# Kernel optimization log

Hardware: AMD Instinct MI355X
Metric: run time of the kernel (lower is better)

Reference implementation:

```python
import jax, jax.numpy as jnp
import numpy as np

WS = 8          # window size
DIM = 512       # channels
NH = 16         # heads
HD = DIM // NH  # head dim = 32
N = WS * WS     # tokens per window = 64
NW = 64         # windows per image
B = 16          # images
BW = B * NW     # total windows = 1024
SCALE = HD ** -0.5


def _relative_position_index():
    # Swin relative position index, shape (N, N), values in [0, (2*WS-1)^2)
    coords = np.stack(np.meshgrid(np.arange(WS), np.arange(WS), indexing='ij'))  # (2, WS, WS)
    coords_flat = coords.reshape(2, -1)                                           # (2, N)
    rel = coords_flat[:, :, None] - coords_flat[:, None, :]                       # (2, N, N)
    rel = rel.transpose(1, 2, 0).astype(np.int32)                                 # (N, N, 2)
    rel[:, :, 0] += WS - 1
    rel[:, :, 1] += WS - 1
    rel[:, :, 0] *= 2 * WS - 1
    return jnp.asarray(rel.sum(-1))                                               # (N, N)


def setup_inputs() -> dict:
    key = jax.random.key(0)
    ks = jax.random.split(key, 7)
    x = jax.random.normal(ks[0], (BW, N, DIM), dtype=jnp.float32)
    mask = jax.random.normal(ks[1], (NW, N, N), dtype=jnp.float32)  # shift mask (additive)
    qkv_w = jax.random.normal(ks[2], (3 * DIM, DIM), dtype=jnp.float32) * 0.02
    qkv_b = jax.random.normal(ks[3], (3 * DIM,), dtype=jnp.float32) * 0.02
    rel_bias_table = jax.random.normal(ks[4], ((2 * WS - 1) ** 2, NH), dtype=jnp.float32) * 0.02
    proj_w = jax.random.normal(ks[5], (DIM, DIM), dtype=jnp.float32) * 0.02
    proj_b = jax.random.normal(ks[6], (DIM,), dtype=jnp.float32) * 0.02
    rel_index = _relative_position_index()
    return {"x": x, "mask": mask, "qkv_w": qkv_w, "qkv_b": qkv_b,
            "rel_bias_table": rel_bias_table, "proj_w": proj_w, "proj_b": proj_b,
            "rel_index": rel_index}


def reference(x, mask, qkv_w, qkv_b, rel_bias_table, proj_w, proj_b, rel_index):
    # qkv projection: (BW, N, 3*DIM) -> (3, BW, NH, N, HD)
    qkv = (x @ qkv_w.T + qkv_b).reshape(BW, N, 3, NH, HD).transpose(2, 0, 3, 1, 4)
    q, k, v = qkv[0], qkv[1], qkv[2]
    # scaled dot-product scores: (BW, NH, N, N)
    attn = jnp.einsum('bhnd,bhmd->bhnm', q * SCALE, k)
    # relative position bias: gather (N*N,) -> (N, N, NH) -> (NH, N, N)
    bias = rel_bias_table[rel_index.reshape(-1)].reshape(N, N, NH).transpose(2, 0, 1)
    attn = attn + bias[None]
    # shift mask: broadcast over images and heads
    attn = attn.reshape(B, NW, NH, N, N) + mask[None, :, None]
    attn = jax.nn.softmax(attn.reshape(BW, NH, N, N), axis=-1)
    # weighted values: (BW, NH, N, HD) -> (BW, N, DIM)
    out = jnp.einsum('bhnm,bhmd->bhnd', attn, v).transpose(0, 2, 1, 3).reshape(BW, N, DIM)
    return out @ proj_w.T + proj_b
```

## Files before the change

kernel.cpp:

```cpp
#include <hip/hip_runtime.h>
#include <hip/hip_bf16.h>

typedef __bf16 bf16;
typedef __bf16 bf16x4 __attribute__((ext_vector_type(4)));
typedef __bf16 bf16x8 __attribute__((ext_vector_type(8)));
typedef float  f32x4  __attribute__((ext_vector_type(4)));

#define AS1 __attribute__((address_space(1)))
#define AS3 __attribute__((address_space(3)))

__device__ __forceinline__ void gld_lds16(const void* g, void* l) {
    __builtin_amdgcn_global_load_lds((AS1 void*)g, (AS3 void*)l, 16, 0, 0);
}

__global__ void cvt_kernel(const float* __restrict__ in, bf16* __restrict__ out,
                           int n4) {
    for (long i = (long)blockIdx.x * blockDim.x + threadIdx.x; i < n4;
         i += (long)gridDim.x * blockDim.x) {
        f32x4 v = ((const f32x4*)in)[i];
        bf16x4 h;
#pragma unroll
        for (int e = 0; e < 4; ++e) h[e] = (bf16)v[e];
        ((bf16x4*)out)[i] = h;
    }
}

__global__ void bmr_kernel(const int* __restrict__ rel_index,
                           const float* __restrict__ table,
                           const float* __restrict__ mask,
                           float* __restrict__ bmr) {
    const float LOG2E = 1.4426950408889634f;
    int idx = blockIdx.x * 256 + threadIdx.x;
    int tj  = idx & 3;
    int r16 = (idx >> 2) & 15;
    int row = (idx >> 6) & 63;
    int h   = (idx >> 12) & 15;
    int nw  = idx >> 16;
    int col = tj * 16 + r16;
    bmr[idx] = (table[rel_index[row * 64 + col] * 16 + h]
                + mask[nw * 4096 + row * 64 + col]) * LOG2E;
}

#define STAGE(GBASE, LBASE, SK0)                                          \
    { _Pragma("unroll")                                                   \
      for (int c_ = 0; c_ < 2; ++c_)                                      \
          gld_lds16((GBASE) + c_ * 16 * 512 + (SK0),                      \
                    (LBASE) + (w * 2 + c_) * 512); }

#define FRAG_A(DST, S, KK, IH)                                              \
  { const bf16* ap_ = sA + ((S)*2+(KK))*8192 + (wm128+(IH)*64+r16)*32 + cq8;\
    _Pragma("unroll")                                                       \
    for (int ii_ = 0; ii_ < 4; ++ii_)                                       \
        DST[ii_] = *(const bf16x8*)(ap_ + ii_*512); }

#define FRAG_B(DST, S, KK)                                                  \
  { const bf16* bp_ = sB + ((S)*2+(KK))*8192 + (wn64+r16)*32 + cq8;         \
    _Pragma("unroll")                                                       \
    for (int jj_ = 0; jj_ < 4; ++jj_)                                       \
        DST[jj_] = *(const bf16x8*)(bp_ + jj_*512); }

#define PH(PFAD, PFS, PFKK, PFIH, PFB, PFBD, GB, LB, SK0, LGK, UAV, UBV,    \
           UIH, VMA)                                                        \
  { FRAG_A(PFAD, PFS, PFKK, PFIH);                                          \
    if (PFB) FRAG_B(PFBD, PFS, PFKK);                                       \
    STAGE(GB, LB, SK0);                                                     \
    __builtin_amdgcn_sched_barrier(0);                                      \
    __builtin_amdgcn_s_barrier();                                           \
    asm volatile("s_waitcnt lgkmcnt(" #LGK ")");                            \
    __builtin_amdgcn_sched_barrier(0);                                      \
    __builtin_amdgcn_s_setprio(1);                                          \
    _Pragma("unroll")                                                       \
    for (int ii_ = 0; ii_ < 4; ++ii_)                                       \
      _Pragma("unroll")                                                     \
      for (int jj_ = 0; jj_ < 4; ++jj_)                                     \
        acc[(UIH)*4+ii_][jj_] = __builtin_amdgcn_mfma_f32_16x16x32_bf16(    \
            UAV[ii_], UBV[jj_], acc[(UIH)*4+ii_][jj_], 0, 0, 0);            \
    __builtin_amdgcn_s_setprio(0);                                          \
    asm volatile(VMA);                                                      \
    __builtin_amdgcn_sched_barrier(0);                                      \
    __builtin_amdgcn_s_barrier(); }

#define GEMM_PREAMBLE                                                       \
    __shared__ __attribute__((aligned(16))) char smemraw[131072];           \
    bf16* sA = (bf16*)smemraw;                                              \
    bf16* sB = sA + 32768;                                                  \
    const int t     = threadIdx.x;                                          \
    const int w     = t >> 6;                                               \
    const int lane  = t & 63;                                               \
    const int q     = lane >> 4;                                            \
    const int r16   = lane & 15;                                            \
    const int wm128 = (w >> 2) * 128;                                       \
    const int wn64  = (w & 3) * 64;                                         \
    const int sc8   = (((lane & 3) ^ ((lane >> 4) & 3)) << 3);              \
    const int cq8   = ((q ^ ((r16 >> 2) & 3)) << 3);

#define GEMM_MAIN(ABASE, BBASE)                                             \
    const bf16* Ast = (ABASE) + (bM + w * 32 + (lane >> 2)) * 512 + sc8;    \
    const bf16* Bst = (BBASE) + (bN + w * 32 + (lane >> 2)) * 512 + sc8;    \
    f32x4 acc[8][4];                                                        \
    _Pragma("unroll")                                                       \
    for (int i = 0; i < 8; ++i)                                             \
        _Pragma("unroll")                                                   \
        for (int j = 0; j < 4; ++j) acc[i][j] = f32x4{0.f, 0.f, 0.f, 0.f};  \
    bf16x8 avA[4], avB[4], bvA[4], bvB[4];                                  \
    STAGE(Ast, sA + 0,     0);                                              \
    STAGE(Bst, sB + 0,     0);                                              \
    STAGE(Ast, sA + 8192,  32);                                             \
    STAGE(Bst, sB + 8192,  32);                                             \
    STAGE(Ast, sA + 16384, 64);                                             \
    STAGE(Bst, sB + 16384, 64);                                             \
    asm volatile("s_waitcnt vmcnt(4)");                                     \
    __builtin_amdgcn_sched_barrier(0);                                      \
    __builtin_amdgcn_s_barrier();                                           \
    FRAG_A(avA, 0, 0, 0);                                                   \
    FRAG_B(bvA, 0, 0);                                                      \
    for (int i = 0; i < 4; ++i) {                                           \
        const int t1 = 2 * i + 1;                                           \
        const int t2 = (2 * i + 2 < 8) ? 2 * i + 2 : 7;                     \
        const int t3 = (2 * i + 3 < 8) ? 2 * i + 3 : 7;                     \
        PH(avB,0,0,1, 0,bvB, Ast, sA+24576, t1*64+32, 4, avA,bvA,0, "")     \
        PH(avA,0,1,1, 1,bvB, Bst, sB+24576, t1*64+32, 8, avB,bvA,1, "")     \
        PH(avB,0,1,0, 0,bvA, Ast, sA+0,     t2*64,    4, avA,bvB,1,         \
           "s_waitcnt vmcnt(6)")                                            \
        PH(avA,1,0,0, 1,bvA, Bst, sB+0,     t2*64,    8, avB,bvB,0, "")     \
        PH(avB,1,0,1, 0,bvB, Ast, sA+8192,  t2*64+32, 4, avA,bvA,0,         \
           "s_waitcnt vmcnt(6)")                                            \
        PH(avA,1,1,1, 1,bvB, Bst, sB+8192,  t2*64+32, 8, avB,bvA,1, "")     \
        PH(avB,1,1,0, 0,bvA, Ast, sA+16384, t3*64,    4, avA,bvB,1,         \
           "s_waitcnt vmcnt(6)")                                            \
        PH(avA,0,0,0, 1,bvA, Bst, sB+16384, t3*64,    8, avB,bvB,0,         \
           "s_waitcnt vmcnt(4)")                                            \
    }                                                                       \
    asm volatile("s_waitcnt vmcnt(0) lgkmcnt(0)");                          \
    __builtin_amdgcn_sched_barrier(0);                                      \
    __builtin_amdgcn_s_barrier();

__global__ __launch_bounds__(512, 2) void gemm1_qkv8(
    const bf16* __restrict__ A, const bf16* __restrict__ B,
    const float* __restrict__ bias, bf16* __restrict__ Cq,
    bf16* __restrict__ Ckv)
{
    GEMM_PREAMBLE
    const int bid = blockIdx.x;
    const int wg  = (bid & 7) * 192 + (bid >> 3);
    const long bM = (long)(wg / 6) * 256;
    const long bN = (long)(wg % 6) * 256;

    GEMM_MAIN(A, B)

    const bool isQ = (bN < 512);
    const float sc = isQ ? 0.25503486f : 1.0f;
    bf16* ct = (bf16*)smemraw;
#pragma unroll
    for (int j = 0; j < 4; ++j) {
        const int col  = wn64 + j * 16 + r16;
        const float bvv = bias[bN + col];
        const int chunk = col >> 3, cl = col & 7;
#pragma unroll
        for (int i = 0; i < 8; ++i)
#pragma unroll
            for (int r = 0; r < 4; ++r) {
                const int row = wm128 + i * 16 + q * 4 + r;
                ct[row * 256 + ((chunk ^ ((row >> 2) & 7)) << 3) + cl] =
                    (bf16)((acc[i][j][r] + bvv) * sc);
            }
    }
    __syncthreads();

    bf16* __restrict__ outp = isQ ? (Cq + bM * 512 + bN)
                                  : (Ckv + bM * 1024 + (bN - 512));
    const int ostr = isQ ? 512 : 1024;
#pragma unroll
    for (int it = 0; it < 16; ++it) {
        const int row = w * 32 + it * 2 + (lane >> 5);
        const int c   = lane & 31;
        uint4 v = *(const uint4*)(ct + row * 256 +
                                  ((c ^ ((row >> 2) & 7)) << 3));
        *(uint4*)(outp + (long)row * ostr + c * 8) = v;
    }
}

__global__ __launch_bounds__(512, 2) void gemm2_proj8(
    const bf16* __restrict__ A, const bf16* __restrict__ B,
    const float* __restrict__ bias, float* __restrict__ C)
{
    GEMM_PREAMBLE
    const int bid = blockIdx.x;
    const int wg  = (bid & 7) * 64 + (bid >> 3);
    const long bM = (long)(wg >> 1) * 256;
    const long bN = (long)(wg & 1) * 256;

    GEMM_MAIN(A, B)

    float* ct32 = (float*)smemraw;
#pragma unroll
    for (int half = 0; half < 2; ++half) {
        __syncthreads();
        if ((w >> 2) == half) {
#pragma unroll
            for (int j = 0; j < 4; ++j) {
                const int col  = wn64 + j * 16 + r16;
                const float bvv = bias[bN + col];
#pragma unroll
                for (int i = 0; i < 8; ++i)
#pragma unroll
                    for (int r = 0; r < 4; ++r) {
                        const int row = i * 16 + q * 4 + r;
                        ct32[row * 256 + (col ^ (((row >> 2) & 7) << 2))] =
                            acc[i][j][r] + bvv;
                    }
            }
        }
        __syncthreads();
#pragma unroll
        for (int it = 0; it < 16; ++it) {
            const int row = it * 8 + w;
            f32x4 v = *(const f32x4*)&ct32[row * 256 +
                                           ((lane * 4) ^ (((row >> 2) & 7) << 2))];
            *(f32x4*)(C + (bM + half * 128 + row) * 512L + bN + lane * 4) = v;
        }
    }
}

__global__ __launch_bounds__(256) void attn_kernel4(
    bf16* __restrict__ qbuf, const bf16* __restrict__ kv,
    const float* __restrict__ bmr)
{
    __shared__ __attribute__((aligned(16))) bf16 smem[24576];
    const int t    = threadIdx.x;
    const int wv   = t >> 6;
    const int lane = t & 63;
    const int q    = lane >> 4;
    const int r16  = lane & 15;
    const int bw   = blockIdx.x >> 2;
    const int hg   = blockIdx.x & 3;
    const int h    = hg * 4 + wv;
    const int nw   = bw & 63;
    const long rowbase = (long)bw * 64;

    bf16* Qs = smem + wv * 6144;
    bf16* Ks = Qs + 2048;
    bf16* Vt = Qs + 4096;
    bf16* Ps = Qs;

    const int sc8 = (((lane & 3) ^ ((lane >> 4) & 3)) << 3);
#pragma unroll
    for (int it = 0; it < 4; ++it) {
        const int tok = it * 16 + (lane >> 2);
        gld_lds16(qbuf + (rowbase + tok) * 512  + h * 32 + sc8, Qs + it * 512);
        gld_lds16(kv   + (rowbase + tok) * 1024 + h * 32 + sc8, Ks + it * 512);
    }
    {
        const bf16* gv = kv + (rowbase + lane) * 1024 + 512 + h * 32;
        uint4 vtmp[4];
#pragma unroll
        for (int jj = 0; jj < 4; ++jj) vtmp[jj] = ((const uint4*)gv)[jj];
        const bf16* vrow = (const bf16*)vtmp;
        const int tchunk = lane >> 3, tin = lane & 7;
#pragma unroll
        for (int hd = 0; hd < 32; ++hd)
            Vt[hd * 64 + ((tchunk ^ (hd & 7)) << 3) + tin] = vrow[hd];
    }
    asm volatile("s_waitcnt vmcnt(0)" ::: "memory");

    const int cq8 = ((q ^ ((r16 >> 2) & 3)) << 3);
    f32x4 acc[4][4];
    {
        bf16x8 av[4], bv[4];
#pragma unroll
        for (int ti = 0; ti < 4; ++ti)
            av[ti] = *(const bf16x8*)&Qs[(ti * 16 + r16) * 32 + cq8];
#pragma unroll
        for (int tj = 0; tj < 4; ++tj)
            bv[tj] = *(const bf16x8*)&Ks[(tj * 16 + r16) * 32 + cq8];
        const f32x4 z = f32x4{0.f, 0.f, 0.f, 0.f};
#pragma unroll
        for (int ti = 0; ti < 4; ++ti)
#pragma unroll
            for (int tj = 0; tj < 4; ++tj)
                acc[ti][tj] = __builtin_amdgcn_mfma_f32_16x16x32_bf16(
                    av[ti], bv[tj], z, 0, 0, 0);
    }

    const float* bmw = bmr + ((long)(nw * 16 + h) << 12);
#pragma unroll
    for (int ti = 0; ti < 4; ++ti) {
        f32x4 bm4[4];
#pragma unroll
        for (int r = 0; r < 4; ++r)
            bm4[r] = *(const f32x4*)(bmw + (ti * 16 + q * 4 + r) * 64 + r16 * 4);
#pragma unroll
        for (int r = 0; r < 4; ++r) {
            const int row = ti * 16 + q * 4 + r;
            float mx = -1e30f;
#pragma unroll
            for (int tj = 0; tj < 4; ++tj) {
                float s = acc[ti][tj][r] + bm4[r][tj];
                acc[ti][tj][r] = s;
                mx = fmaxf(mx, s);
            }
#pragma unroll
            for (int d = 1; d < 16; d <<= 1)
                mx = fmaxf(mx, __shfl_xor(mx, d, 16));
            float sum = 0.f;
#pragma unroll
            for (int tj = 0; tj < 4; ++tj) {
                float e = exp2f(acc[ti][tj][r] - mx);
                acc[ti][tj][r] = e;
                sum += e;
            }
#pragma unroll
            for (int d = 1; d < 16; d <<= 1)
                sum += __shfl_xor(sum, d, 16);
            const float inv = 1.0f / sum;
#pragma unroll
            for (int tj = 0; tj < 4; ++tj) {
                const int c = tj * 16 + r16;
                Ps[row * 64 + ((((c >> 3) ^ (row & 7)) << 3) + (c & 7))] =
                    (bf16)(acc[ti][tj][r] * inv);
            }
        }
    }

    f32x4 o[4][2];
#pragma unroll
    for (int ti = 0; ti < 4; ++ti)
#pragma unroll
        for (int tn = 0; tn < 2; ++tn)
            o[ti][tn] = f32x4{0.f, 0.f, 0.f, 0.f};

#pragma unroll
    for (int ks = 0; ks < 2; ++ks) {
        bf16x8 av[4], bv[2];
        const int ch = (((ks * 4 + q) ^ (r16 & 7)) << 3);
#pragma unroll
        for (int ti = 0; ti < 4; ++ti)
            av[ti] = *(const bf16x8*)&Ps[(ti * 16 + r16) * 64 + ch];
#pragma unroll
        for (int tn = 0; tn < 2; ++tn)
            bv[tn] = *(const bf16x8*)&Vt[(tn * 16 + r16) * 64 + ch];
#pragma unroll
        for (int ti = 0; ti < 4; ++ti)
#pragma unroll
            for (int tn = 0; tn < 2; ++tn)
                o[ti][tn] = __builtin_amdgcn_mfma_f32_16x16x32_bf16(
                    av[ti], bv[tn], o[ti][tn], 0, 0, 0);
    }

#pragma unroll
    for (int ti = 0; ti < 4; ++ti)
#pragma unroll
        for (int tn = 0; tn < 2; ++tn)
#pragma unroll
            for (int r = 0; r < 4; ++r)
                Qs[(ti * 16 + q * 4 + r) * 32 + tn * 16 + r16] =
                    (bf16)(o[ti][tn][r]);
    __syncthreads();

    bf16* op = qbuf + rowbase * 512 + hg * 128;
#pragma unroll
    for (int it = 0; it < 4; ++it) {
        const int idx = it * 256 + t;
        const int row = idx >> 4;
        const int c   = idx & 15;
        const int hl  = c >> 2;
        uint4 v = *(const uint4*)(smem + hl * 6144 + row * 32 + (c & 3) * 8);
        *(uint4*)(op + (long)row * 512 + hl * 32 + (c & 3) * 8) = v;
    }
}

extern "C" void kernel_launch(void* const* d_in, const int* in_sizes, int n_in,
                              void* d_out, int out_size, void* d_ws, size_t ws_size,
                              hipStream_t stream) {
    const float* x      = (const float*)d_in[0];
    const float* mask   = (const float*)d_in[1];
    const float* qkv_w  = (const float*)d_in[2];
    const float* qkv_b  = (const float*)d_in[3];
    const float* table  = (const float*)d_in[4];
    const float* proj_w = (const float*)d_in[5];
    const float* proj_b = (const float*)d_in[6];
    const int*   relidx = (const int*)d_in[7];
    float* out = (float*)d_out;

    char*  ws   = (char*)d_ws;
    bf16*  qbuf = (bf16*)(ws + 262144);
    bf16*  xbf  = (bf16*)(ws + 67371008);
    float* bmr  = (float*)(ws + 67371008);
    bf16*  wq   = (bf16*)(ws + 134479872);
    bf16*  wp   = (bf16*)(ws + 136052736);
    const size_t need_full = 136577024ull + 134217728ull;
    bf16* kvbuf = (ws_size >= need_full) ? (bf16*)(ws + 136577024)
                                         : (bf16*)d_out;

    cvt_kernel<<<2048, 256, 0, stream>>>(x,      xbf, 8388608);
    cvt_kernel<<<768,  256, 0, stream>>>(qkv_w,  wq,  196608);
    cvt_kernel<<<256,  256, 0, stream>>>(proj_w, wp,  65536);

    gemm1_qkv8<<<1536, 512, 0, stream>>>(xbf, wq, qkv_b, qbuf, kvbuf);
    bmr_kernel<<<16384, 256, 0, stream>>>(relidx, table, mask, bmr);
    attn_kernel4<<<4096, 256, 0, stream>>>(qbuf, kvbuf, bmr);
    gemm2_proj8<<<512, 512, 0, stream>>>(qbuf, wp, proj_b, out);
}
```

Before: 531.5 us.

## Compute transposed scores K·Qᵀ so softmax rows reduce with fewer shuffles

```diff
diff --git a/kernel.cpp b/kernel.cpp
--- a/kernel.cpp
+++ b/kernel.cpp
@@ -31,12 +31,14 @@
                            float* __restrict__ bmr) {
     const float LOG2E = 1.4426950408889634f;
     int idx = blockIdx.x * 256 + threadIdx.x;
-    int tj  = idx & 3;
-    int r16 = (idx >> 2) & 15;
-    int row = (idx >> 6) & 63;
+    int r   = idx & 3;
+    int ln  = (idx >> 2) & 63;
+    int tk  = (idx >> 8) & 3;
+    int tq  = (idx >> 10) & 3;
     int h   = (idx >> 12) & 15;
     int nw  = idx >> 16;
-    int col = tj * 16 + r16;
+    int row = tq * 16 + (ln & 15);
+    int col = tk * 16 + (ln >> 4) * 4 + r;
     bmr[idx] = (table[rel_index[row * 64 + col] * 16 + h]
                 + mask[nw * 4096 + row * 64 + col]) * LOG2E;
 }
@@ -243,6 +245,11 @@
     bf16* Vt = Qs + 4096;
     bf16* Ps = Qs;
 
+    const bf16* gv = kv + (rowbase + lane) * 1024 + 512 + h * 32;
+    uint4 vtmp[4];
+#pragma unroll
+    for (int jj = 0; jj < 4; ++jj) vtmp[jj] = ((const uint4*)gv)[jj];
+
     const int sc8 = (((lane & 3) ^ ((lane >> 4) & 3)) << 3);
 #pragma unroll
     for (int it = 0; it < 4; ++it) {
@@ -251,10 +258,6 @@
         gld_lds16(kv   + (rowbase + tok) * 1024 + h * 32 + sc8, Ks + it * 512);
     }
     {
-        const bf16* gv = kv + (rowbase + lane) * 1024 + 512 + h * 32;
-        uint4 vtmp[4];
-#pragma unroll
-        for (int jj = 0; jj < 4; ++jj) vtmp[jj] = ((const uint4*)gv)[jj];
         const bf16* vrow = (const bf16*)vtmp;
         const int tchunk = lane >> 3, tin = lane & 7;
 #pragma unroll
@@ -266,59 +269,58 @@
     const int cq8 = ((q ^ ((r16 >> 2) & 3)) << 3);
     f32x4 acc[4][4];
     {
-        bf16x8 av[4], bv[4];
-#pragma unroll
-        for (int ti = 0; ti < 4; ++ti)
-            av[ti] = *(const bf16x8*)&Qs[(ti * 16 + r16) * 32 + cq8];
-#pragma unroll
-        for (int tj = 0; tj < 4; ++tj)
-            bv[tj] = *(const bf16x8*)&Ks[(tj * 16 + r16) * 32 + cq8];
+        bf16x8 kf[4], qf[4];
+#pragma unroll
+        for (int tk = 0; tk < 4; ++tk)
+            kf[tk] = *(const bf16x8*)&Ks[(tk * 16 + r16) * 32 + cq8];
+#pragma unroll
+        for (int tq = 0; tq < 4; ++tq)
+            qf[tq] = *(const bf16x8*)&Qs[(tq * 16 + r16) * 32 + cq8];
         const f32x4 z = f32x4{0.f, 0.f, 0.f, 0.f};
 #pragma unroll
-        for (int ti = 0; ti < 4; ++ti)
-#pragma unroll
-            for (int tj = 0; tj < 4; ++tj)
-                acc[ti][tj] = __builtin_amdgcn_mfma_f32_16x16x32_bf16(
-                    av[ti], bv[tj], z, 0, 0, 0);
+        for (int tk = 0; tk < 4; ++tk)
+#pragma unroll
+            for (int tq = 0; tq < 4; ++tq)
+                acc[tk][tq] = __builtin_amdgcn_mfma_f32_16x16x32_bf16(
+                    kf[tk], qf[tq], z, 0, 0, 0);
     }
 
     const float* bmw = bmr + ((long)(nw * 16 + h) << 12);
 #pragma unroll
-    for (int ti = 0; ti < 4; ++ti) {
-        f32x4 bm4[4];
-#pragma unroll
-        for (int r = 0; r < 4; ++r)
-            bm4[r] = *(const f32x4*)(bmw + (ti * 16 + q * 4 + r) * 64 + r16 * 4);
-#pragma unroll
-        for (int r = 0; r < 4; ++r) {
-            const int row = ti * 16 + q * 4 + r;
-            float mx = -1e30f;
-#pragma unroll
-            for (int tj = 0; tj < 4; ++tj) {
-                float s = acc[ti][tj][r] + bm4[r][tj];
-                acc[ti][tj][r] = s;
-                mx = fmaxf(mx, s);
-            }
-#pragma unroll
-            for (int d = 1; d < 16; d <<= 1)
-                mx = fmaxf(mx, __shfl_xor(mx, d, 16));
-            float sum = 0.f;
-#pragma unroll
-            for (int tj = 0; tj < 4; ++tj) {
-                float e = exp2f(acc[ti][tj][r] - mx);
-                acc[ti][tj][r] = e;
+    for (int tq = 0; tq < 4; ++tq) {
+        f32x4 s[4];
+#pragma unroll
+        for (int tk = 0; tk < 4; ++tk)
+            s[tk] = acc[tk][tq]
+                  + *(const f32x4*)(bmw + ((tq * 4 + tk) * 64 + lane) * 4);
+        float mx = -1e30f;
+#pragma unroll
+        for (int tk = 0; tk < 4; ++tk)
+#pragma unroll
+            for (int r = 0; r < 4; ++r) mx = fmaxf(mx, s[tk][r]);
+        mx = fmaxf(mx, __shfl_xor(mx, 16));
+        mx = fmaxf(mx, __shfl_xor(mx, 32));
+        float sum = 0.f;
+#pragma unroll
+        for (int tk = 0; tk < 4; ++tk)
+#pragma unroll
+            for (int r = 0; r < 4; ++r) {
+                float e = exp2f(s[tk][r] - mx);
+                s[tk][r] = e;
                 sum += e;
             }
-#pragma unroll
-            for (int d = 1; d < 16; d <<= 1)
-                sum += __shfl_xor(sum, d, 16);
-            const float inv = 1.0f / sum;
-#pragma unroll
-            for (int tj = 0; tj < 4; ++tj) {
-                const int c = tj * 16 + r16;
-                Ps[row * 64 + ((((c >> 3) ^ (row & 7)) << 3) + (c & 7))] =
-                    (bf16)(acc[ti][tj][r] * inv);
-            }
+        sum += __shfl_xor(sum, 16);
+        sum += __shfl_xor(sum, 32);
+        const float inv = 1.0f / sum;
+        const int qrow = tq * 16 + r16;
+#pragma unroll
+        for (int tk = 0; tk < 4; ++tk) {
+            bf16x4 pv;
+#pragma unroll
+            for (int r = 0; r < 4; ++r) pv[r] = (bf16)(s[tk][r] * inv);
+            *(bf16x4*)&Ps[qrow * 64 +
+                          (((tk * 2 + (q >> 1)) ^ (qrow & 7)) << 3) +
+                          (q & 1) * 4] = pv;
         }
     }
 
```

Measured after the change: 515.3 us. 1.03x faster.
